# Performance work log

Measured on AMD Instinct MI355X. Metric: run time of the kernel, lower is better.

The kernel has to match this reference:

```python
import jax, jax.numpy as jnp
import numpy as np

DIM_IN = 1024
DIM_OUT = 1024
B = 8192


def setup_inputs() -> dict:
    key = jax.random.key(0)
    ks = jax.random.split(key, 8)
    d = DIM_IN + DIM_OUT
    bound = 1.0 / np.sqrt(d)
    def lin(kw, kb):
        W = jax.random.uniform(kw, (d, DIM_OUT), jnp.float32, -bound, bound)
        b = jax.random.uniform(kb, (DIM_OUT,), jnp.float32, -bound, bound)
        return W, b
    kx, kh, kc, kp = ks[0], ks[1], ks[2], ks[3]
    pw = jax.random.split(kp, 8)
    W_I, b_I = lin(pw[0], pw[1])
    W_F, b_F = lin(pw[2], pw[3])
    W_G, b_G = lin(pw[4], pw[5])
    W_O, b_O = lin(pw[6], pw[7])
    return {
        "x": jax.random.normal(kx, (B, DIM_IN), jnp.float32),
        "h": jax.random.normal(kh, (B, DIM_OUT), jnp.float32),
        "c": jax.random.normal(kc, (B, DIM_OUT), jnp.float32),
        "W_I": W_I, "b_I": b_I,
        "W_F": W_F, "b_F": b_F,
        "W_G": W_G, "b_G": b_G,
        "W_O": W_O, "b_O": b_O,
    }


def reference(x, h, c, W_I, b_I, W_F, b_F, W_G, b_G, W_O, b_O):
    X = jnp.concatenate([x, h], axis=-1)  # [B, dimIn+dimOut]
    # Fuse the 4 gate projections into one GEMM: [B,d] @ [d, 4*dimOut]
    W = jnp.concatenate([W_I, W_F, W_G, W_O], axis=1)
    b = jnp.concatenate([b_I, b_F, b_G, b_O], axis=0)
    gates = X @ W + b
    i_, f_, g_, o_ = jnp.split(gates, 4, axis=-1)
    I = jax.nn.sigmoid(i_)
    F = jax.nn.sigmoid(f_)
    G = jnp.tanh(g_)
    O = jax.nn.sigmoid(o_)
    C = F * c + I * G
    return O * jnp.tanh(C), C
```

## Files before the change

### kernel.cpp

```cpp
#include <hip/hip_runtime.h>
#include <cstdint>


#define B_ROWS 8192
#define DK 2048
#define DOUT 1024
#define TM 128
#define TN 128
#define BK 32

typedef __bf16 bf16x8 __attribute__((ext_vector_type(8)));
typedef __bf16 bf16x4 __attribute__((ext_vector_type(4)));
typedef float f32x4 __attribute__((ext_vector_type(4)));

__device__ inline void load16_to_lds(const __bf16* gsrc, __bf16* ldst) {
    __builtin_amdgcn_global_load_lds(
        (const __attribute__((address_space(1))) void*)gsrc,
        (__attribute__((address_space(3))) void*)ldst,
        16, 0, 0);
}

__device__ inline float sigmoidf_fast(float x) {
    return 1.0f / (1.0f + __expf(-x));
}

__global__ __launch_bounds__(256) void prep_x(const float* __restrict__ x,
                                              const float* __restrict__ h,
                                              __bf16* __restrict__ X) {
    int id = blockIdx.x * 256 + threadIdx.x;
    int b = id >> 9;
    int k = (id & 511) * 4;
    float4 v;
    if (k < 1024) v = *(const float4*)&x[(size_t)b * 1024 + k];
    else          v = *(const float4*)&h[(size_t)b * 1024 + (k - 1024)];
    bf16x4 o = { (__bf16)v.x, (__bf16)v.y, (__bf16)v.z, (__bf16)v.w };
    *(bf16x4*)&X[(size_t)b * 2048 + k] = o;
}

__global__ __launch_bounds__(256) void prep_w(const float* __restrict__ WI,
                                              const float* __restrict__ WF,
                                              const float* __restrict__ WG,
                                              const float* __restrict__ WO,
                                              __bf16* __restrict__ Wt) {
    int kb = blockIdx.x;
    int nb = blockIdx.y;
    int g = nb & 3;
    int j0 = (nb >> 2) * 32;
    const float* W = (g == 0) ? WI : (g == 1) ? WF : (g == 2) ? WG : WO;
    __shared__ float t[32][33];
    int tx = threadIdx.x, ty0 = threadIdx.y;
    for (int yy = 0; yy < 32; yy += 8) {
        int k = kb * 32 + ty0 + yy;
        t[ty0 + yy][tx] = W[(size_t)k * 1024 + j0 + tx];
    }
    __syncthreads();
    for (int yy = 0; yy < 32; yy += 8) {
        int row = ty0 + yy;
        int np = nb * 32 + row;
        Wt[(size_t)np * 2048 + kb * 32 + tx] = (__bf16)t[tx][row];
    }
}

__global__ __launch_bounds__(256) void lstm_gemm(
    const __bf16* __restrict__ Xbf, const __bf16* __restrict__ Wt,
    const float* __restrict__ c,
    const float* __restrict__ bI, const float* __restrict__ bF,
    const float* __restrict__ bG, const float* __restrict__ bO,
    float* __restrict__ outH, float* __restrict__ outC)
{
    __shared__ __bf16 As[TM * BK];
    __shared__ __bf16 Bs[TN * BK];

    const int t = threadIdx.x;
    const int lane = t & 63;
    const int wave = t >> 6;
    const int m0 = blockIdx.x * TM;
    const int nb = blockIdx.y;
    const int n0 = nb * TN;

    f32x4 acc[2][8];
#pragma unroll
    for (int i = 0; i < 2; ++i)
#pragma unroll
        for (int j = 0; j < 8; ++j) acc[i][j] = (f32x4){0.f, 0.f, 0.f, 0.f};

    const int r0 = t >> 2, kc0 = (t & 3) * 8;
    const int r1 = (256 + t) >> 2, kc1 = kc0;
    const __bf16* gA0 = Xbf + (size_t)(m0 + r0) * DK + kc0;
    const __bf16* gA1 = Xbf + (size_t)(m0 + r1) * DK + kc1;
    const __bf16* gB0 = Wt + (size_t)(n0 + r0) * DK + kc0;
    const __bf16* gB1 = Wt + (size_t)(n0 + r1) * DK + kc1;
    __bf16* lA0 = As + wave * 512;
    __bf16* lA1 = As + 2048 + wave * 512;
    __bf16* lB0 = Bs + wave * 512;
    __bf16* lB1 = Bs + 2048 + wave * 512;

    const int lr = lane & 15;
    const int kh = (lane >> 4) * 8;

    for (int kk = 0; kk < DK / BK; ++kk) {
        load16_to_lds(gA0, lA0);
        load16_to_lds(gA1, lA1);
        load16_to_lds(gB0, lB0);
        load16_to_lds(gB1, lB1);
        gA0 += BK; gA1 += BK; gB0 += BK; gB1 += BK;
        __syncthreads();

        bf16x8 a0 = *(const bf16x8*)&As[(wave * 32 + lr) * BK + kh];
        bf16x8 a1 = *(const bf16x8*)&As[(wave * 32 + 16 + lr) * BK + kh];
        bf16x8 bb[8];
#pragma unroll
        for (int j = 0; j < 8; ++j)
            bb[j] = *(const bf16x8*)&Bs[(j * 16 + lr) * BK + kh];
#pragma unroll
        for (int j = 0; j < 8; ++j) {
            acc[0][j] = __builtin_amdgcn_mfma_f32_16x16x32_bf16(a0, bb[j], acc[0][j], 0, 0, 0);
            acc[1][j] = __builtin_amdgcn_mfma_f32_16x16x32_bf16(a1, bb[j], acc[1][j], 0, 0, 0);
        }
        __syncthreads();
    }

    const int col = lane & 15;
    const int rbase = m0 + wave * 32 + (lane >> 4) * 4;
#pragma unroll
    for (int i = 0; i < 2; ++i) {
#pragma unroll
        for (int p = 0; p < 2; ++p) {
            int j = nb * 32 + p * 16 + col;
            float biI = bI[j], biF = bF[j], biG = bG[j], biO = bO[j];
#pragma unroll
            for (int r = 0; r < 4; ++r) {
                int row = rbase + i * 16 + r;
                float vI = acc[i][0 + p][r] + biI;
                float vF = acc[i][2 + p][r] + biF;
                float vG = acc[i][4 + p][r] + biG;
                float vO = acc[i][6 + p][r] + biO;
                float I = sigmoidf_fast(vI);
                float F = sigmoidf_fast(vF);
                float G = tanhf(vG);
                float O = sigmoidf_fast(vO);
                size_t idx = (size_t)row * DOUT + j;
                float Cn = F * c[idx] + I * G;
                outH[idx] = O * tanhf(Cn);
                outC[idx] = Cn;
            }
        }
    }
}

extern "C" void kernel_launch(void* const* d_in, const int* in_sizes, int n_in,
                              void* d_out, int out_size, void* d_ws, size_t ws_size,
                              hipStream_t stream) {
    const float* x  = (const float*)d_in[0];
    const float* h  = (const float*)d_in[1];
    const float* c  = (const float*)d_in[2];
    const float* WI = (const float*)d_in[3];
    const float* bI = (const float*)d_in[4];
    const float* WF = (const float*)d_in[5];
    const float* bF = (const float*)d_in[6];
    const float* WG = (const float*)d_in[7];
    const float* bG = (const float*)d_in[8];
    const float* WO = (const float*)d_in[9];
    const float* bO = (const float*)d_in[10];

    __bf16* Xbf = (__bf16*)d_ws;
    __bf16* Wt  = (__bf16*)((char*)d_ws + (size_t)B_ROWS * DK * 2);
    float* outH = (float*)d_out;
    float* outC = outH + (size_t)B_ROWS * DOUT;

    prep_x<<<(B_ROWS * DK / 4) / 256, 256, 0, stream>>>(x, h, Xbf);
    prep_w<<<dim3(DK / 32, 4 * DOUT / 32), dim3(32, 8), 0, stream>>>(WI, WF, WG, WO, Wt);
    lstm_gemm<<<dim3(B_ROWS / TM, 4 * DOUT / TN), 256, 0, stream>>>(
        Xbf, Wt, c, bI, bF, bG, bO, outH, outC);
}
```

Baseline: 378.5 us.

## Use 2x2 wave tiling with gate-interleaved weight layout and fast activations

Each wave now computes a 64x64 sub-tile instead of a 32x128 strip. Per k-step it loads 4 A and 4 B fragments rather than 2 A and 8 B, which cuts LDS reads relative to the MFMA count. The weight prep kernel reorders columns so each 16-column group holds one gate, letting each wave's four B fragments map to I/F/G/O for the same output columns. Sigmoid and tanh are rewritten with hardware exp2 and rcp intrinsics, which trades a little accuracy for fewer instructions in the epilogue.

```diff
diff --git a/kernel.cpp b/kernel.cpp
--- a/kernel.cpp
+++ b/kernel.cpp
@@ -20,8 +20,11 @@
         16, 0, 0);
 }
 
-__device__ inline float sigmoidf_fast(float x) {
-    return 1.0f / (1.0f + __expf(-x));
+__device__ inline float fast_sigmoid(float x) {
+    return __builtin_amdgcn_rcpf(1.0f + __builtin_amdgcn_exp2f(-1.442695041f * x));
+}
+__device__ inline float fast_tanh(float x) {
+    return 1.0f - 2.0f * __builtin_amdgcn_rcpf(1.0f + __builtin_amdgcn_exp2f(2.885390082f * x));
 }
 
 __global__ __launch_bounds__(256) void prep_x(const float* __restrict__ x,
@@ -43,21 +46,27 @@
                                               const float* __restrict__ WO,
                                               __bf16* __restrict__ Wt) {
     int kb = blockIdx.x;
-    int nb = blockIdx.y;
-    int g = nb & 3;
-    int j0 = (nb >> 2) * 32;
-    const float* W = (g == 0) ? WI : (g == 1) ? WF : (g == 2) ? WG : WO;
+    int jb = blockIdx.y;
+    int j0 = jb * 32;
     __shared__ float t[32][33];
-    int tx = threadIdx.x, ty0 = threadIdx.y;
-    for (int yy = 0; yy < 32; yy += 8) {
-        int k = kb * 32 + ty0 + yy;
-        t[ty0 + yy][tx] = W[(size_t)k * 1024 + j0 + tx];
-    }
-    __syncthreads();
-    for (int yy = 0; yy < 32; yy += 8) {
-        int row = ty0 + yy;
-        int np = nb * 32 + row;
-        Wt[(size_t)np * 2048 + kb * 32 + tx] = (__bf16)t[tx][row];
+    int tx = threadIdx.x, ty = threadIdx.y;
+    const float* Ws[4] = {WI, WF, WG, WO};
+#pragma unroll
+    for (int g = 0; g < 4; ++g) {
+        const float* W = Ws[g];
+#pragma unroll
+        for (int yy = 0; yy < 32; yy += 8) {
+            int k = kb * 32 + ty + yy;
+            t[ty + yy][tx] = W[(size_t)k * 1024 + j0 + tx];
+        }
+        __syncthreads();
+#pragma unroll
+        for (int yy = 0; yy < 32; yy += 8) {
+            int r = ty + yy;
+            int npp = (jb * 2 + (r >> 4)) * 64 + g * 16 + (r & 15);
+            Wt[(size_t)npp * 2048 + kb * 32 + tx] = (__bf16)t[tx][r];
+        }
+        __syncthreads();
     }
 }
 
@@ -74,22 +83,24 @@
     const int t = threadIdx.x;
     const int lane = t & 63;
     const int wave = t >> 6;
+    const int wm = wave >> 1;
+    const int wn = wave & 1;
     const int m0 = blockIdx.x * TM;
     const int nb = blockIdx.y;
     const int n0 = nb * TN;
 
-    f32x4 acc[2][8];
+    f32x4 acc[4][4];
 #pragma unroll
-    for (int i = 0; i < 2; ++i)
+    for (int i = 0; i < 4; ++i)
 #pragma unroll
-        for (int j = 0; j < 8; ++j) acc[i][j] = (f32x4){0.f, 0.f, 0.f, 0.f};
+        for (int j = 0; j < 4; ++j) acc[i][j] = (f32x4){0.f, 0.f, 0.f, 0.f};
 
     const int r0 = t >> 2, kc0 = (t & 3) * 8;
-    const int r1 = (256 + t) >> 2, kc1 = kc0;
+    const int r1 = 64 + r0;
     const __bf16* gA0 = Xbf + (size_t)(m0 + r0) * DK + kc0;
-    const __bf16* gA1 = Xbf + (size_t)(m0 + r1) * DK + kc1;
+    const __bf16* gA1 = Xbf + (size_t)(m0 + r1) * DK + kc0;
     const __bf16* gB0 = Wt + (size_t)(n0 + r0) * DK + kc0;
-    const __bf16* gB1 = Wt + (size_t)(n0 + r1) * DK + kc1;
+    const __bf16* gB1 = Wt + (size_t)(n0 + r1) * DK + kc0;
     __bf16* lA0 = As + wave * 512;
     __bf16* lA1 = As + 2048 + wave * 512;
     __bf16* lB0 = Bs + wave * 512;
@@ -97,6 +108,8 @@
 
     const int lr = lane & 15;
     const int kh = (lane >> 4) * 8;
+    const int arow = wm * 64 + lr;
+    const int brow = wn * 64 + lr;
 
     for (int kk = 0; kk < DK / BK; ++kk) {
         load16_to_lds(gA0, lA0);
@@ -106,44 +119,38 @@
         gA0 += BK; gA1 += BK; gB0 += BK; gB1 += BK;
         __syncthreads();
 
-        bf16x8 a0 = *(const bf16x8*)&As[(wave * 32 + lr) * BK + kh];
-        bf16x8 a1 = *(const bf16x8*)&As[(wave * 32 + 16 + lr) * BK + kh];
-        bf16x8 bb[8];
+        bf16x8 a[4], b[4];
 #pragma unroll
-        for (int j = 0; j < 8; ++j)
-            bb[j] = *(const bf16x8*)&Bs[(j * 16 + lr) * BK + kh];
+        for (int i = 0; i < 4; ++i)
+            a[i] = *(const bf16x8*)&As[(arow + i * 16) * BK + kh];
 #pragma unroll
-        for (int j = 0; j < 8; ++j) {
-            acc[0][j] = __builtin_amdgcn_mfma_f32_16x16x32_bf16(a0, bb[j], acc[0][j], 0, 0, 0);
-            acc[1][j] = __builtin_amdgcn_mfma_f32_16x16x32_bf16(a1, bb[j], acc[1][j], 0, 0, 0);
-        }
+        for (int j = 0; j < 4; ++j)
+            b[j] = *(const bf16x8*)&Bs[(brow + j * 16) * BK + kh];
+#pragma unroll
+        for (int i = 0; i < 4; ++i)
+#pragma unroll
+            for (int j = 0; j < 4; ++j)
+                acc[i][j] = __builtin_amdgcn_mfma_f32_16x16x32_bf16(a[i], b[j], acc[i][j], 0, 0, 0);
         __syncthreads();
     }
 
     const int col = lane & 15;
-    const int rbase = m0 + wave * 32 + (lane >> 4) * 4;
+    const int j = (nb * 2 + wn) * 16 + col;
+    const float biI = bI[j], biF = bF[j], biG = bG[j], biO = bO[j];
+    const int rbase = m0 + wm * 64 + (lane >> 4) * 4;
 #pragma unroll
-    for (int i = 0; i < 2; ++i) {
+    for (int i = 0; i < 4; ++i) {
 #pragma unroll
-        for (int p = 0; p < 2; ++p) {
-            int j = nb * 32 + p * 16 + col;
-            float biI = bI[j], biF = bF[j], biG = bG[j], biO = bO[j];
-#pragma unroll
-            for (int r = 0; r < 4; ++r) {
-                int row = rbase + i * 16 + r;
-                float vI = acc[i][0 + p][r] + biI;
-                float vF = acc[i][2 + p][r] + biF;
-                float vG = acc[i][4 + p][r] + biG;
-                float vO = acc[i][6 + p][r] + biO;
-                float I = sigmoidf_fast(vI);
-                float F = sigmoidf_fast(vF);
-                float G = tanhf(vG);
-                float O = sigmoidf_fast(vO);
-                size_t idx = (size_t)row * DOUT + j;
-                float Cn = F * c[idx] + I * G;
-                outH[idx] = O * tanhf(Cn);
-                outC[idx] = Cn;
-            }
+        for (int r = 0; r < 4; ++r) {
+            int row = rbase + i * 16 + r;
+            float I = fast_sigmoid(acc[i][0][r] + biI);
+            float F = fast_sigmoid(acc[i][1][r] + biF);
+            float G = fast_tanh(acc[i][2][r] + biG);
+            float O = fast_sigmoid(acc[i][3][r] + biO);
+            size_t idx = (size_t)row * DOUT + j;
+            float Cn = F * c[idx] + I * G;
+            outH[idx] = O * fast_tanh(Cn);
+            outC[idx] = Cn;
         }
     }
 }
@@ -169,7 +176,7 @@
     float* outC = outH + (size_t)B_ROWS * DOUT;
 
     prep_x<<<(B_ROWS * DK / 4) / 256, 256, 0, stream>>>(x, h, Xbf);
-    prep_w<<<dim3(DK / 32, 4 * DOUT / 32), dim3(32, 8), 0, stream>>>(WI, WF, WG, WO, Wt);
+    prep_w<<<dim3(DK / 32, DOUT / 32), dim3(32, 8), 0, stream>>>(WI, WF, WG, WO, Wt);
     lstm_gemm<<<dim3(B_ROWS / TM, 4 * DOUT / TN), 256, 0, stream>>>(
         Xbf, Wt, c, bI, bF, bG, bO, outH, outC);
 }
```

New measurement: 357.7 us. -5.5%, faster.
